# Kernel tuning notes

Hardware: AMD Instinct MI355X
Metric: run time of the kernel (lower is better)

The kernel has to match this reference:

```python
import jax, jax.numpy as jnp
import numpy as np

DEPTH_REF = jnp.array([28.01, 16.32], dtype=jnp.float32)
DIM_REF = jnp.array([[3.88, 1.63, 1.53], [0.84, 1.76, 0.66], [1.78, 1.52, 1.78]], dtype=jnp.float32)
TOPK = 50
DET_THRESHOLD = 0.25
PI = 3.14159265358979


def nms_hm(heat, kernel=3):
    # 3x3 max-pool NMS: keep peaks, zero everything else
    pad = (kernel - 1) // 2
    hmax = jax.lax.reduce_window(heat, -jnp.inf, jax.lax.max,
                                 (1, 1, kernel, kernel), (1, 1, 1, 1),
                                 [(0, 0), (0, 0), (pad, pad), (pad, pad)])
    return jnp.where(hmax == heat, heat, 0.0)


def select_topk(heat, K):
    B, C, H, W = heat.shape
    scores_all, inds_all = jax.lax.top_k(heat.reshape(B, C, H * W), K)  # [B,C,K]
    ys_all = (inds_all // W).astype(jnp.float32)
    xs_all = (inds_all % W).astype(jnp.float32)
    scores, inds = jax.lax.top_k(scores_all.reshape(B, C * K), K)       # [B,K] over classes
    clses = (inds // K).astype(jnp.float32)
    topk_inds = jnp.take_along_axis(inds_all.reshape(B, C * K), inds, axis=1)
    ys = jnp.take_along_axis(ys_all.reshape(B, C * K), inds, axis=1)
    xs = jnp.take_along_axis(xs_all.reshape(B, C * K), inds, axis=1)
    return scores, topk_inds, clses, ys, xs


def select_point_of_interest(index, feature_maps):
    B, Cf, H, W = feature_maps.shape
    fm = feature_maps.transpose(0, 2, 3, 1).reshape(B, H * W, Cf)
    return jnp.take_along_axis(fm, index[:, :, None], axis=1)  # [B,K,Cf]


def encode_box3d(rotys, dims, locs):
    # dims = (l, h, w); corner signs reproduce SMOKE's gather pattern
    N = rotys.shape[0]
    c, s = jnp.cos(rotys), jnp.sin(rotys)
    z, o = jnp.zeros_like(c), jnp.ones_like(c)
    ry = jnp.stack([c, z, s, z, o, z, -s, z, c], axis=1).reshape(N, 3, 3)
    sx = jnp.array([-0.5, 0.5, 0.5, 0.5, 0.5, -0.5, -0.5, -0.5], dtype=dims.dtype)
    sy = jnp.array([-1., -1., 0., 0., -1., -1., 0., 0.], dtype=dims.dtype)
    sz = jnp.array([-0.5, -0.5, -0.5, 0.5, 0.5, 0.5, 0.5, -0.5], dtype=dims.dtype)
    corners = jnp.stack([dims[:, 0:1] * sx, dims[:, 1:2] * sy, dims[:, 2:3] * sz], axis=1)  # [N,3,8]
    return jnp.einsum('nij,njk->nik', ry, corners) + locs[:, :, None]


def setup_inputs() -> dict:
    key = jax.random.key(0)
    k1, k2 = jax.random.split(key)
    B, C, H, W = 32, 3, 192, 640
    IMG_W, IMG_H = 4 * W, 4 * H
    pred_heatmap = jax.random.uniform(k1, (B, C, H, W), dtype=jnp.float32)
    pred_regression = jax.random.normal(k2, (B, 8, H, W), dtype=jnp.float32) * 0.5
    # affine image->heatmap (scale 1/4), invertible
    tm = jnp.array([[0.25, 0., 0.], [0., 0.25, 0.], [0., 0., 1.]], dtype=jnp.float32)
    trans_mat = jnp.tile(tm[None], (B, 1, 1))
    Kc = jnp.array([[721.5, 0., IMG_W / 2.], [0., 721.5, IMG_H / 2.], [0., 0., 1.]], dtype=jnp.float32)
    K_mat = jnp.tile(Kc[None], (B, 1, 1))
    img_size = jnp.tile(jnp.array([[IMG_W, IMG_H]], dtype=jnp.float32), (B, 1))
    return {"pred_heatmap": pred_heatmap, "pred_regression": pred_regression,
            "trans_mat": trans_mat, "K_mat": K_mat, "img_size": img_size}


def reference(pred_heatmap, pred_regression, trans_mat, K_mat, img_size):
    B = pred_heatmap.shape[0]
    heat = nms_hm(pred_heatmap)
    scores, inds, clses, ys, xs = select_topk(heat, TOPK)
    reg = select_point_of_interest(inds, pred_regression).reshape(-1, 8)  # [B*K,8]

    points = jnp.stack([xs.reshape(-1), ys.reshape(-1)], axis=1)          # heatmap coords
    depth_off, proj_off = reg[:, 0], reg[:, 1:3]
    dim_off, ori = reg[:, 3:6], reg[:, 6:8]
    cls_idx = clses.reshape(-1).astype(jnp.int32)

    obj_id = jnp.repeat(jnp.arange(B), TOPK)
    tm_inv = jnp.linalg.inv(trans_mat)[obj_id]   # [N,3,3]
    K_inv = jnp.linalg.inv(K_mat)[obj_id]

    # decode location: heatmap -> image -> camera frame
    proj = points + proj_off
    proj_ext = jnp.concatenate([proj, jnp.ones_like(proj[:, :1])], axis=1)
    proj_img = jnp.einsum('nij,nj->ni', tm_inv, proj_ext)                 # image-plane homog coords
    depths = depth_off * DEPTH_REF[1] + DEPTH_REF[0]
    locs = jnp.einsum('nij,nj->ni', K_inv, proj_img * depths[:, None])

    dims = jnp.exp(dim_off) * DIM_REF[cls_idx]                            # (l,h,w)
    locs = locs.at[:, 1].add(dims[:, 1] / 2)

    # decode orientation
    eps = 1e-7
    rays = jnp.arctan(locs[:, 0] / (locs[:, 2] + eps))
    alphas = jnp.arctan(ori[:, 0] / (ori[:, 1] + eps))
    alphas = jnp.where(ori[:, 1] >= 0, alphas - PI / 2, alphas + PI / 2)
    rotys = alphas + rays
    wrap = lambda a: jnp.where(a > PI, a - 2 * PI, jnp.where(a < -PI, a + 2 * PI, a))
    rotys, alphas = wrap(rotys), wrap(alphas)

    # encode 2D boxes from projected 3D corners
    corners = encode_box3d(rotys, dims, locs)                             # [N,3,8]
    proj2 = jnp.einsum('nij,njk->nik', K_mat[obj_id], corners)
    xy = proj2[:, :2] / proj2[:, 2:3]
    Wi, Hi = img_size[obj_id, 0], img_size[obj_id, 1]
    xmins = jnp.clip(xy[:, 0].min(axis=1), 0.0, Wi)
    ymins = jnp.clip(xy[:, 1].min(axis=1), 0.0, Hi)
    xmaxs = jnp.clip(xy[:, 0].max(axis=1), 0.0, Wi)
    ymaxs = jnp.clip(xy[:, 1].max(axis=1), 0.0, Hi)
    box2d = jnp.stack([xmins, ymins, xmaxs, ymaxs], axis=1)

    dims_rolled = jnp.roll(dims, -1, axis=1)                              # (h,w,l)
    result = jnp.concatenate([
        cls_idx.astype(jnp.float32)[:, None], alphas[:, None], box2d,
        dims_rolled, locs, rotys[:, None], scores.reshape(-1, 1)], axis=1)  # [B*K,14]
    keep = result[:, -1] > DET_THRESHOLD
    return jnp.where(keep[:, None], result, 0.0)
```

## Files before the change

kernel.cpp:

```cpp
#include <hip/hip_runtime.h>
#include <math.h>

#define Hd 192
#define Wd 640
#define HWp (Hd * Wd)
#define NCLS 3
#define KTOP 50
#define NB 32
#define NPL (NB * NCLS)
#define GPR 160
#define GPP (HWp / 4)
#define SPR 40
#define SEGBLK 30
#define SEGCAP 64
#define CAP 2048
#define RBK 256
#define PI_F 3.14159265358979f

__device__ inline float fmax3(float a, float b, float c) {
  return fmaxf(fmaxf(a, b), c);
}

template <typename F>
__device__ inline void peaks_in_group(const float* __restrict__ p, int g, F&& f) {
  const int y = g / GPR;
  const int x0 = (g - y * GPR) * 4;
  const float* rm = p + y * Wd + x0;
  const float4 mq = *(const float4*)rm;
  const float ml = (x0 > 0) ? rm[-1] : -INFINITY;
  const float mr = (x0 + 4 < Wd) ? rm[4] : -INFINITY;
  float4 tq; float tl, tr;
  if (y > 0) {
    const float* rt = rm - Wd;
    tq = *(const float4*)rt;
    tl = (x0 > 0) ? rt[-1] : -INFINITY;
    tr = (x0 + 4 < Wd) ? rt[4] : -INFINITY;
  } else {
    tq.x = tq.y = tq.z = tq.w = -INFINITY; tl = -INFINITY; tr = -INFINITY;
  }
  float4 bq; float bl, br;
  if (y < Hd - 1) {
    const float* rb = rm + Wd;
    bq = *(const float4*)rb;
    bl = (x0 > 0) ? rb[-1] : -INFINITY;
    br = (x0 + 4 < Wd) ? rb[4] : -INFINITY;
  } else {
    bq.x = bq.y = bq.z = bq.w = -INFINITY; bl = -INFINITY; br = -INFINITY;
  }
  const float c0 = fmax3(tl, ml, bl);
  const float c1 = fmax3(tq.x, mq.x, bq.x);
  const float c2 = fmax3(tq.y, mq.y, bq.y);
  const float c3 = fmax3(tq.z, mq.z, bq.z);
  const float c4 = fmax3(tq.w, mq.w, bq.w);
  const float c5 = fmax3(tr, mr, br);
  const int base = y * Wd + x0;
  if (mq.x == fmax3(c0, c1, c2)) f(__float_as_uint(mq.x), base + 0);
  if (mq.y == fmax3(c1, c2, c3)) f(__float_as_uint(mq.y), base + 1);
  if (mq.z == fmax3(c2, c3, c4)) f(__float_as_uint(mq.z), base + 2);
  if (mq.w == fmax3(c3, c4, c5)) f(__float_as_uint(mq.w), base + 3);
}

template <typename F>
__device__ inline void for_each_peak_plane(const float* __restrict__ p, int tid,
                                           int nth, F&& f) {
  for (int g = tid; g < GPP; g += nth) peaks_in_group(p, g, f);
}

__device__ inline unsigned long long mk_key(unsigned int bits, int idx) {
  return ((unsigned long long)bits << 32) | (unsigned int)~idx;
}

__device__ inline int bucket_of(unsigned int bits) {
  const unsigned int base = __float_as_uint(0.995f);
  if (bits <= base) return 0;
  unsigned int d = (bits - base) >> 9;
  return d > 255u ? 255 : (int)d;
}

struct Row16 {
  float4 q0, q1, q2, q3;
  float l, r;
};

__device__ inline Row16 load_row16(const float* __restrict__ rp, int x0, bool valid) {
  Row16 o;
  if (valid) {
    o.q0 = *(const float4*)(rp);
    o.q1 = *(const float4*)(rp + 4);
    o.q2 = *(const float4*)(rp + 8);
    o.q3 = *(const float4*)(rp + 12);
    o.l = (x0 > 0) ? rp[-1] : -INFINITY;
    o.r = (x0 + 16 < Wd) ? rp[16] : -INFINITY;
  } else {
    o.q0.x = o.q0.y = o.q0.z = o.q0.w = -INFINITY;
    o.q1 = o.q0; o.q2 = o.q0; o.q3 = o.q0;
    o.l = -INFINITY; o.r = -INFINITY;
  }
  return o;
}

__device__ inline float4 max3v(const float4 a, const float4 b, const float4 c) {
  float4 o;
  o.x = fmax3(a.x, b.x, c.x);
  o.y = fmax3(a.y, b.y, c.y);
  o.z = fmax3(a.z, b.z, c.z);
  o.w = fmax3(a.w, b.w, c.w);
  return o;
}

__global__ __launch_bounds__(256) void scan_kernel(
    const float* __restrict__ heat,
    int* __restrict__ counts,
    unsigned long long* __restrict__ segkey) {
  const int blk = blockIdx.x;
  const int plane = blk / SEGBLK;
  const int sub = blk - plane * SEGBLK;
  __shared__ unsigned long long s_k[SEGCAP];
  __shared__ int s_n;
  if (threadIdx.x == 0) s_n = 0;
  __syncthreads();

  const int strip = sub * 256 + threadIdx.x;
  const int y = strip / SPR;
  const int x0 = (strip - y * SPR) * 16;
  const float* pm = heat + (size_t)plane * HWp + y * Wd + x0;

  const Row16 m = load_row16(pm, x0, true);
  const Row16 t = load_row16(pm - Wd, x0, y > 0);
  const Row16 b = load_row16(pm + Wd, x0, y < Hd - 1);

  const float cl = fmax3(t.l, m.l, b.l);
  const float cr = fmax3(t.r, m.r, b.r);
  const float4 c0 = max3v(t.q0, m.q0, b.q0);
  const float4 c1 = max3v(t.q1, m.q1, b.q1);
  const float4 c2 = max3v(t.q2, m.q2, b.q2);
  const float4 c3 = max3v(t.q3, m.q3, b.q3);

  const float TH = 0.995f;
  const int base = y * Wd + x0;
#define EMIT(V, W0, W1, W2, J)                                         \
  if ((V) >= TH && (V) == fmax3((W0), (W1), (W2))) {                   \
    int slot = atomicAdd(&s_n, 1);                                     \
    if (slot < SEGCAP) s_k[slot] = mk_key(__float_as_uint(V), base + (J)); \
  }
  EMIT(m.q0.x, cl,   c0.x, c0.y, 0)
  EMIT(m.q0.y, c0.x, c0.y, c0.z, 1)
  EMIT(m.q0.z, c0.y, c0.z, c0.w, 2)
  EMIT(m.q0.w, c0.z, c0.w, c1.x, 3)
  EMIT(m.q1.x, c0.w, c1.x, c1.y, 4)
  EMIT(m.q1.y, c1.x, c1.y, c1.z, 5)
  EMIT(m.q1.z, c1.y, c1.z, c1.w, 6)
  EMIT(m.q1.w, c1.z, c1.w, c2.x, 7)
  EMIT(m.q2.x, c1.w, c2.x, c2.y, 8)
  EMIT(m.q2.y, c2.x, c2.y, c2.z, 9)
  EMIT(m.q2.z, c2.y, c2.z, c2.w, 10)
  EMIT(m.q2.w, c2.z, c2.w, c3.x, 11)
  EMIT(m.q3.x, c2.w, c3.x, c3.y, 12)
  EMIT(m.q3.y, c3.x, c3.y, c3.z, 13)
  EMIT(m.q3.z, c3.y, c3.z, c3.w, 14)
  EMIT(m.q3.w, c3.z, c3.w, cr,   15)
#undef EMIT

  __syncthreads();
  const int n = s_n;
  if (threadIdx.x == 0) counts[blk] = n;
  const int nn = n < SEGCAP ? n : SEGCAP;
  if (threadIdx.x < nn)
    segkey[(size_t)blk * SEGCAP + threadIdx.x] = s_k[threadIdx.x];
}

__device__ inline void inv3(const float* m, float* o) {
  float a = m[0], b = m[1], c = m[2];
  float d = m[3], e = m[4], f = m[5];
  float g = m[6], h = m[7], i = m[8];
  float A = e * i - f * h;
  float B = -(d * i - f * g);
  float C = d * h - e * g;
  float det = a * A + b * B + c * C;
  float id = 1.0f / det;
  o[0] = A * id;            o[1] = -(b * i - c * h) * id; o[2] = (b * f - c * e) * id;
  o[3] = B * id;            o[4] = (a * i - c * g) * id;  o[5] = -(a * f - c * d) * id;
  o[6] = C * id;            o[7] = -(a * h - b * g) * id; o[8] = (a * e - b * d) * id;
}

__device__ inline float wrap_pi(float a) {
  if (a > PI_F) return a - 2.0f * PI_F;
  if (a < -PI_F) return a + 2.0f * PI_F;
  return a;
}

__constant__ float DIM_REF_C[9] = {3.88f, 1.63f, 1.53f,
                                   0.84f, 1.76f, 0.66f,
                                   1.78f, 1.52f, 1.78f};

__global__ __launch_bounds__(768) void rank3_decode_kernel(
    const float* __restrict__ heat,
    const int* __restrict__ counts,
    const unsigned long long* __restrict__ segkey,
    const float* __restrict__ regr,
    const float* __restrict__ trans_mat,
    const float* __restrict__ K_mat,
    const float* __restrict__ img_size,
    float* __restrict__ out) {
  const int b = blockIdx.x;
  const int tid = threadIdx.x;
  const int g = tid >> 8;
  const int t = tid & 255;

  __shared__ unsigned long long s_key[NCLS][CAP];
  __shared__ unsigned long long g_key[NCLS][CAP];
  __shared__ int s_off[NCLS][SEGBLK + 1];
  __shared__ int cnt[NCLS][RBK], suf[NCLS][RBK], cur[NCLS][RBK];
  __shared__ unsigned int fb_hist[1024];
  __shared__ float cls_sc[NCLS * KTOP];
  __shared__ int cls_pi[NCLS * KTOP];
  __shared__ int sel[KTOP];
  __shared__ int s_flag[NCLS], s_M[NCLS], s_fast[NCLS], s_all_fast;
  __shared__ int fb_cnt, fb_B, fb_above, fb_T;

  const int plane = b * NCLS + g;

  if (tid == 0) s_all_fast = 1;
  if (t == 0) { s_flag[g] = 0; s_off[g][0] = 0; }
  __syncthreads();
  if (t < SEGBLK) {
    int n = counts[plane * SEGBLK + t];
    if (n > SEGCAP) { atomicOr(&s_flag[g], 1); n = SEGCAP; }
    s_off[g][t + 1] = n;
  }
  __syncthreads();
  if (t == 0) {
    int acc = 0;
    for (int i = 1; i <= SEGBLK; ++i) { acc += s_off[g][i]; s_off[g][i] = acc; }
    s_M[g] = acc;
    const int fast = (s_flag[g] == 0) && (acc >= KTOP) && (acc <= CAP);
    s_fast[g] = fast;
    if (!fast) s_all_fast = 0;
  }
  __syncthreads();

  if (s_all_fast) {
    const unsigned long long* pk = segkey + (size_t)plane * SEGBLK * SEGCAP;
    for (int i = t; i < SEGBLK * SEGCAP; i += 256) {
      const int s = i >> 6;
      const int j = i & (SEGCAP - 1);
      const int o = s_off[g][s];
      const int n = s_off[g][s + 1] - o;
      if (j < n) s_key[g][o + j] = pk[(size_t)s * SEGCAP + j];
    }
  } else {
    for (int p = 0; p < NCLS; ++p) {
      if (s_fast[p]) {
        const unsigned long long* pk =
            segkey + (size_t)(b * NCLS + p) * SEGBLK * SEGCAP;
        for (int i = tid; i < SEGBLK * SEGCAP; i += 768) {
          const int s = i >> 6;
          const int j = i & (SEGCAP - 1);
          const int o = s_off[p][s];
          const int n = s_off[p][s + 1] - o;
          if (j < n) s_key[p][o + j] = pk[(size_t)s * SEGCAP + j];
        }
        __syncthreads();
      } else {
        const float* hp = heat + (size_t)(b * NCLS + p) * HWp;
        for (int i = tid; i < 1024; i += 768) fb_hist[i] = 0;
        __syncthreads();
        for_each_peak_plane(hp, tid, 768, [&](unsigned int bits, int idx) {
          unsigned int bkt = bits >> 20; if (bkt > 1023u) bkt = 1023u;
          atomicAdd(&fb_hist[bkt], 1u);
        });
        __syncthreads();
        if (tid == 0) {
          int acc = 0, Bs = -1;
          for (int bkt = 1023; bkt >= 0; --bkt) {
            int cc = (int)fb_hist[bkt];
            if (acc + cc >= KTOP) { Bs = bkt; fb_above = acc; break; }
            acc += cc;
          }
          fb_B = Bs;
          if (Bs < 0) fb_above = acc;
        }
        __syncthreads();
        const int Bs = fb_B;
        unsigned int T;
        if (Bs < 0) {
          T = 0;
        } else {
          for (int i = tid; i < 1024; i += 768) fb_hist[i] = 0;
          __syncthreads();
          for_each_peak_plane(hp, tid, 768, [&](unsigned int bits, int idx) {
            unsigned int bkt = bits >> 20; if (bkt > 1023u) bkt = 1023u;
            if ((int)bkt == Bs) atomicAdd(&fb_hist[(bits >> 10) & 1023], 1u);
          });
          __syncthreads();
          if (tid == 0) {
            int acc = fb_above, Ss = 0;
            for (int sb = 1023; sb >= 0; --sb) {
              int cc = (int)fb_hist[sb];
              if (acc + cc >= KTOP) { Ss = sb; break; }
              acc += cc;
            }
            fb_T = (int)(((unsigned int)Bs << 20) | ((unsigned int)Ss << 10));
          }
          __syncthreads();
          T = (unsigned int)fb_T;
        }
        if (tid == 0) fb_cnt = 0;
        __syncthreads();
        for_each_peak_plane(hp, tid, 768, [&](unsigned int bits, int idx) {
          if (bits >= T) {
            int slot = atomicAdd(&fb_cnt, 1);
            if (slot < CAP) s_key[p][slot] = mk_key(bits, idx);
          }
        });
        __syncthreads();
        if (tid == 0) s_M[p] = fb_cnt < CAP ? fb_cnt : CAP;
        __syncthreads();
      }
    }
  }
  __syncthreads();
  const int M = s_M[g];

  for (int i = t; i < RBK; i += 256) { cnt[g][i] = 0; cur[g][i] = 0; }
  __syncthreads();
  for (int i = t; i < M; i += 256)
    atomicAdd(&cnt[g][bucket_of((unsigned int)(s_key[g][i] >> 32))], 1);
  __syncthreads();
  if (t == 0) {
    int acc = 0;
    for (int bq = RBK - 1; bq >= 0; --bq) { suf[g][bq] = acc; acc += cnt[g][bq]; }
  }
  __syncthreads();
  for (int i = t; i < M; i += 256) {
    const unsigned long long k = s_key[g][i];
    const int bq = bucket_of((unsigned int)(k >> 32));
    const int slot = suf[g][bq] + atomicAdd(&cur[g][bq], 1);
    g_key[g][slot] = k;
  }
  __syncthreads();
  for (int i = t; i < M; i += 256) {
    const unsigned long long k = g_key[g][i];
    const int bq = bucket_of((unsigned int)(k >> 32));
    const int st = suf[g][bq];
    const int nb = cnt[g][bq];
    int rank = st;
    for (int tt = st; tt < st + nb; ++tt) rank += (g_key[g][tt] > k);
    if (rank < KTOP) {
      cls_sc[g * KTOP + rank] = __uint_as_float((unsigned int)(k >> 32));
      cls_pi[g * KTOP + rank] = (int)~((unsigned int)k);
    }
  }
  for (int s2 = M + t; s2 < KTOP; s2 += 256) {
    cls_sc[g * KTOP + s2] = 0.0f;
    cls_pi[g * KTOP + s2] = 0;
  }
  __syncthreads();

  if (tid < NCLS * KTOP) {
    const float v = cls_sc[tid];
    int rank = 0;
    for (int j = 0; j < NCLS * KTOP; ++j) {
      const float w = cls_sc[j];
      rank += (w > v) || (w == v && j < tid);
    }
    if (rank < KTOP) sel[rank] = tid;
  }
  __syncthreads();

  if (tid < KTOP) {
    const int i = sel[tid];
    const int cls = i / KTOP;
    const float score = cls_sc[i];
    const int ind = cls_pi[i];
    const float ys = (float)(ind / Wd);
    const float xs = (float)(ind - (ind / Wd) * Wd);

    const float* rb = regr + (size_t)b * 8 * HWp + ind;
    const float r0 = rb[0 * HWp], r1 = rb[1 * HWp], r2 = rb[2 * HWp], r3 = rb[3 * HWp];
    const float r4 = rb[4 * HWp], r5 = rb[5 * HWp], r6 = rb[6 * HWp], r7 = rb[7 * HWp];

    float tm[9], km[9], tmi[9], kmi[9];
#pragma unroll
    for (int q = 0; q < 9; ++q) { tm[q] = trans_mat[b * 9 + q]; km[q] = K_mat[b * 9 + q]; }
    inv3(tm, tmi);
    inv3(km, kmi);

    const float px = xs + r1, py = ys + r2;
    const float gx = tmi[0] * px + tmi[1] * py + tmi[2];
    const float gy = tmi[3] * px + tmi[4] * py + tmi[5];
    const float gz = tmi[6] * px + tmi[7] * py + tmi[8];
    const float depth = r0 * 16.32f + 28.01f;
    const float qx = gx * depth, qy = gy * depth, qz = gz * depth;
    const float lx = kmi[0] * qx + kmi[1] * qy + kmi[2] * qz;
    float ly = kmi[3] * qx + kmi[4] * qy + kmi[5] * qz;
    const float lz = kmi[6] * qx + kmi[7] * qy + kmi[8] * qz;

    const float d0 = expf(r3) * DIM_REF_C[cls * 3 + 0];
    const float d1 = expf(r4) * DIM_REF_C[cls * 3 + 1];
    const float d2 = expf(r5) * DIM_REF_C[cls * 3 + 2];
    ly += d1 * 0.5f;

    const float ray = atanf(lx / (lz + 1e-7f));
    float alpha = atanf(r6 / (r7 + 1e-7f));
    alpha += (r7 >= 0.0f) ? -PI_F * 0.5f : PI_F * 0.5f;
    const float roty = wrap_pi(alpha + ray);
    alpha = wrap_pi(alpha);

    const float SX[8] = {-0.5f, 0.5f, 0.5f, 0.5f, 0.5f, -0.5f, -0.5f, -0.5f};
    const float SY[8] = {-1.0f, -1.0f, 0.0f, 0.0f, -1.0f, -1.0f, 0.0f, 0.0f};
    const float SZ[8] = {-0.5f, -0.5f, -0.5f, 0.5f, 0.5f, 0.5f, 0.5f, -0.5f};
    const float cr = cosf(roty), sr = sinf(roty);
    float minx = INFINITY, maxx = -INFINITY, miny = INFINITY, maxy = -INFINITY;
#pragma unroll
    for (int j = 0; j < 8; ++j) {
      const float ax = d0 * SX[j], ay = d1 * SY[j], az = d2 * SZ[j];
      const float cx = cr * ax + sr * az + lx;
      const float cy = ay + ly;
      const float cz = -sr * ax + cr * az + lz;
      const float ppx = km[0] * cx + km[1] * cy + km[2] * cz;
      const float ppy = km[3] * cx + km[4] * cy + km[5] * cz;
      const float ppz = km[6] * cx + km[7] * cy + km[8] * cz;
      const float X = ppx / ppz, Y = ppy / ppz;
      minx = fminf(minx, X); maxx = fmaxf(maxx, X);
      miny = fminf(miny, Y); maxy = fmaxf(maxy, Y);
    }
    const float Wi = img_size[b * 2 + 0], Hi = img_size[b * 2 + 1];
    const float xmin = fminf(fmaxf(minx, 0.0f), Wi);
    const float ymin = fminf(fmaxf(miny, 0.0f), Hi);
    const float xmax = fminf(fmaxf(maxx, 0.0f), Wi);
    const float ymax = fminf(fmaxf(maxy, 0.0f), Hi);

    float* o = out + (size_t)(b * KTOP + tid) * 14;
    if (score > 0.25f) {
      o[0] = (float)cls; o[1] = alpha;
      o[2] = xmin; o[3] = ymin; o[4] = xmax; o[5] = ymax;
      o[6] = d1; o[7] = d2; o[8] = d0;
      o[9] = lx; o[10] = ly; o[11] = lz;
      o[12] = roty; o[13] = score;
    } else {
#pragma unroll
      for (int q = 0; q < 14; ++q) o[q] = 0.0f;
    }
  }
}


extern "C" void kernel_launch(void* const* d_in, const int* in_sizes, int n_in,
                              void* d_out, int out_size, void* d_ws, size_t ws_size,
                              hipStream_t stream) {
  const float* heat = (const float*)d_in[0];
  const float* regr = (const float*)d_in[1];
  const float* tmat = (const float*)d_in[2];
  const float* kmat = (const float*)d_in[3];
  const float* isz = (const float*)d_in[4];

  char* ws = (char*)d_ws;
  int* counts = (int*)ws;
  unsigned long long* segkey = (unsigned long long*)(ws + 16384);

  scan_kernel<<<NPL * SEGBLK, 256, 0, stream>>>(heat, counts, segkey);
  rank3_decode_kernel<<<NB, 768, 0, stream>>>(heat, counts, segkey,
                                              regr, tmat, kmat, isz,
                                              (float*)d_out);
}
```

Measured before the change: 213.4 us.

## Fuse scan and rank/decode into one kernel using last-block-done atomic counters

After: 312.2 us. 1.46x slower.

```diff
diff --git a/kernel.cpp b/kernel.cpp
--- a/kernel.cpp
+++ b/kernel.cpp
@@ -16,6 +16,35 @@
 #define CAP 2048
 #define RBK 256
 #define PI_F 3.14159265358979f
+
+#define OFF_COUNTS 0
+#define OFF_SEGKEY 16384
+#define OFF_PSC 0x200000
+#define OFF_PPI 0x206000
+#define OFF_FLAGS 0x20C000
+
+__device__ inline void g_store_u64(unsigned long long* p, unsigned long long v) {
+  __hip_atomic_store(p, v, __ATOMIC_RELAXED, __HIP_MEMORY_SCOPE_AGENT);
+}
+__device__ inline unsigned long long g_load_u64(const unsigned long long* p) {
+  return __hip_atomic_load((unsigned long long*)p, __ATOMIC_RELAXED,
+                           __HIP_MEMORY_SCOPE_AGENT);
+}
+__device__ inline void g_store_i32(int* p, int v) {
+  __hip_atomic_store(p, v, __ATOMIC_RELAXED, __HIP_MEMORY_SCOPE_AGENT);
+}
+__device__ inline int g_load_i32(const int* p) {
+  return __hip_atomic_load((int*)p, __ATOMIC_RELAXED, __HIP_MEMORY_SCOPE_AGENT);
+}
+__device__ inline void g_store_f32(float* p, float v) {
+  __hip_atomic_store(p, v, __ATOMIC_RELAXED, __HIP_MEMORY_SCOPE_AGENT);
+}
+__device__ inline float g_load_f32(const float* p) {
+  return __hip_atomic_load((float*)p, __ATOMIC_RELAXED, __HIP_MEMORY_SCOPE_AGENT);
+}
+__device__ inline int done_add_acqrel(int* p) {
+  return __hip_atomic_fetch_add(p, 1, __ATOMIC_ACQ_REL, __HIP_MEMORY_SCOPE_AGENT);
+}
 
 __device__ inline float fmax3(float a, float b, float c) {
   return fmaxf(fmaxf(a, b), c);
@@ -108,67 +137,6 @@
   return o;
 }
 
-__global__ __launch_bounds__(256) void scan_kernel(
-    const float* __restrict__ heat,
-    int* __restrict__ counts,
-    unsigned long long* __restrict__ segkey) {
-  const int blk = blockIdx.x;
-  const int plane = blk / SEGBLK;
-  const int sub = blk - plane * SEGBLK;
-  __shared__ unsigned long long s_k[SEGCAP];
-  __shared__ int s_n;
-  if (threadIdx.x == 0) s_n = 0;
-  __syncthreads();
-
-  const int strip = sub * 256 + threadIdx.x;
-  const int y = strip / SPR;
-  const int x0 = (strip - y * SPR) * 16;
-  const float* pm = heat + (size_t)plane * HWp + y * Wd + x0;
-
-  const Row16 m = load_row16(pm, x0, true);
-  const Row16 t = load_row16(pm - Wd, x0, y > 0);
-  const Row16 b = load_row16(pm + Wd, x0, y < Hd - 1);
-
-  const float cl = fmax3(t.l, m.l, b.l);
-  const float cr = fmax3(t.r, m.r, b.r);
-  const float4 c0 = max3v(t.q0, m.q0, b.q0);
-  const float4 c1 = max3v(t.q1, m.q1, b.q1);
-  const float4 c2 = max3v(t.q2, m.q2, b.q2);
-  const float4 c3 = max3v(t.q3, m.q3, b.q3);
-
-  const float TH = 0.995f;
-  const int base = y * Wd + x0;
-#define EMIT(V, W0, W1, W2, J)                                         \
-  if ((V) >= TH && (V) == fmax3((W0), (W1), (W2))) {                   \
-    int slot = atomicAdd(&s_n, 1);                                     \
-    if (slot < SEGCAP) s_k[slot] = mk_key(__float_as_uint(V), base + (J)); \
-  }
-  EMIT(m.q0.x, cl,   c0.x, c0.y, 0)
-  EMIT(m.q0.y, c0.x, c0.y, c0.z, 1)
-  EMIT(m.q0.z, c0.y, c0.z, c0.w, 2)
-  EMIT(m.q0.w, c0.z, c0.w, c1.x, 3)
-  EMIT(m.q1.x, c0.w, c1.x, c1.y, 4)
-  EMIT(m.q1.y, c1.x, c1.y, c1.z, 5)
-  EMIT(m.q1.z, c1.y, c1.z, c1.w, 6)
-  EMIT(m.q1.w, c1.z, c1.w, c2.x, 7)
-  EMIT(m.q2.x, c1.w, c2.x, c2.y, 8)
-  EMIT(m.q2.y, c2.x, c2.y, c2.z, 9)
-  EMIT(m.q2.z, c2.y, c2.z, c2.w, 10)
-  EMIT(m.q2.w, c2.z, c2.w, c3.x, 11)
-  EMIT(m.q3.x, c2.w, c3.x, c3.y, 12)
-  EMIT(m.q3.y, c3.x, c3.y, c3.z, 13)
-  EMIT(m.q3.z, c3.y, c3.z, c3.w, 14)
-  EMIT(m.q3.w, c3.z, c3.w, cr,   15)
-#undef EMIT
-
-  __syncthreads();
-  const int n = s_n;
-  if (threadIdx.x == 0) counts[blk] = n;
-  const int nn = n < SEGCAP ? n : SEGCAP;
-  if (threadIdx.x < nn)
-    segkey[(size_t)blk * SEGCAP + threadIdx.x] = s_k[threadIdx.x];
-}
-
 __device__ inline void inv3(const float* m, float* o) {
   float a = m[0], b = m[1], c = m[2];
   float d = m[3], e = m[4], f = m[5];
@@ -193,175 +161,257 @@
                                    0.84f, 1.76f, 0.66f,
                                    1.78f, 1.52f, 1.78f};
 
-__global__ __launch_bounds__(768) void rank3_decode_kernel(
+__global__ __launch_bounds__(128) void zero_flags_kernel(int* __restrict__ flags) {
+  flags[threadIdx.x] = 0;
+}
+
+__global__ __launch_bounds__(256) void fused_kernel(
     const float* __restrict__ heat,
-    const int* __restrict__ counts,
-    const unsigned long long* __restrict__ segkey,
     const float* __restrict__ regr,
     const float* __restrict__ trans_mat,
     const float* __restrict__ K_mat,
     const float* __restrict__ img_size,
+    int* __restrict__ counts,
+    unsigned long long* __restrict__ segkey,
+    float* __restrict__ plane_sc,
+    int* __restrict__ plane_pi,
+    int* __restrict__ plane_done,
+    int* __restrict__ batch_done,
     float* __restrict__ out) {
-  const int b = blockIdx.x;
+  const int blk = blockIdx.x;
+  const int plane = blk % NPL;
+  const int sub = blk / NPL;
   const int tid = threadIdx.x;
-  const int g = tid >> 8;
-  const int t = tid & 255;
-
-  __shared__ unsigned long long s_key[NCLS][CAP];
-  __shared__ unsigned long long g_key[NCLS][CAP];
-  __shared__ int s_off[NCLS][SEGBLK + 1];
-  __shared__ int cnt[NCLS][RBK], suf[NCLS][RBK], cur[NCLS][RBK];
-  __shared__ unsigned int fb_hist[1024];
-  __shared__ float cls_sc[NCLS * KTOP];
-  __shared__ int cls_pi[NCLS * KTOP];
+
+  __shared__ unsigned long long s_key[CAP];
+  __shared__ unsigned long long c_key[CAP];
+  __shared__ unsigned long long s_k[SEGCAP];
+  __shared__ int s_off[SEGBLK + 1];
+  __shared__ int cnt[RBK], suf[RBK], cur[RBK];
+  __shared__ float d_sc[NCLS * KTOP];
+  __shared__ int d_pi[NCLS * KTOP];
   __shared__ int sel[KTOP];
-  __shared__ int s_flag[NCLS], s_M[NCLS], s_fast[NCLS], s_all_fast;
-  __shared__ int fb_cnt, fb_B, fb_above, fb_T;
-
-  const int plane = b * NCLS + g;
-
-  if (tid == 0) s_all_fast = 1;
-  if (t == 0) { s_flag[g] = 0; s_off[g][0] = 0; }
-  __syncthreads();
-  if (t < SEGBLK) {
-    int n = counts[plane * SEGBLK + t];
-    if (n > SEGCAP) { atomicOr(&s_flag[g], 1); n = SEGCAP; }
-    s_off[g][t + 1] = n;
-  }
-  __syncthreads();
-  if (t == 0) {
+  __shared__ int s_n, s_flag, s_M, s_fast, s_win, s_last;
+  __shared__ int s_fbB, s_fbAbove, s_fbT, s_fbCnt;
+
+  if (tid == 0) s_n = 0;
+  __syncthreads();
+
+  {
+    const int strip = sub * 256 + tid;
+    const int y = strip / SPR;
+    const int x0 = (strip - y * SPR) * 16;
+    const float* pm = heat + (size_t)plane * HWp + y * Wd + x0;
+
+    const Row16 m = load_row16(pm, x0, true);
+    const Row16 t = load_row16(pm - Wd, x0, y > 0);
+    const Row16 bt = load_row16(pm + Wd, x0, y < Hd - 1);
+
+    const float cl = fmax3(t.l, m.l, bt.l);
+    const float cr = fmax3(t.r, m.r, bt.r);
+    const float4 c0 = max3v(t.q0, m.q0, bt.q0);
+    const float4 c1 = max3v(t.q1, m.q1, bt.q1);
+    const float4 c2 = max3v(t.q2, m.q2, bt.q2);
+    const float4 c3 = max3v(t.q3, m.q3, bt.q3);
+
+    const float TH = 0.995f;
+    const int base = y * Wd + x0;
+#define EMIT(V, W0, W1, W2, J)                                         \
+    if ((V) >= TH && (V) == fmax3((W0), (W1), (W2))) {                 \
+      int slot = atomicAdd(&s_n, 1);                                   \
+      if (slot < SEGCAP) s_k[slot] = mk_key(__float_as_uint(V), base + (J)); \
+    }
+    EMIT(m.q0.x, cl,   c0.x, c0.y, 0)
+    EMIT(m.q0.y, c0.x, c0.y, c0.z, 1)
+    EMIT(m.q0.z, c0.y, c0.z, c0.w, 2)
+    EMIT(m.q0.w, c0.z, c0.w, c1.x, 3)
+    EMIT(m.q1.x, c0.w, c1.x, c1.y, 4)
+    EMIT(m.q1.y, c1.x, c1.y, c1.z, 5)
+    EMIT(m.q1.z, c1.y, c1.z, c1.w, 6)
+    EMIT(m.q1.w, c1.z, c1.w, c2.x, 7)
+    EMIT(m.q2.x, c1.w, c2.x, c2.y, 8)
+    EMIT(m.q2.y, c2.x, c2.y, c2.z, 9)
+    EMIT(m.q2.z, c2.y, c2.z, c2.w, 10)
+    EMIT(m.q2.w, c2.z, c2.w, c3.x, 11)
+    EMIT(m.q3.x, c2.w, c3.x, c3.y, 12)
+    EMIT(m.q3.y, c3.x, c3.y, c3.z, 13)
+    EMIT(m.q3.z, c3.y, c3.z, c3.w, 14)
+    EMIT(m.q3.w, c3.z, c3.w, cr,   15)
+#undef EMIT
+  }
+
+  __syncthreads();
+  {
+    const int n = s_n;
+    const int cidx = plane * SEGBLK + sub;
+    if (tid == 0) g_store_i32(&counts[cidx], n);
+    const int nn = n < SEGCAP ? n : SEGCAP;
+    if (tid < nn)
+      g_store_u64(&segkey[(size_t)cidx * SEGCAP + tid], s_k[tid]);
+  }
+  __syncthreads();
+  if (tid == 0) {
+    const int r = done_add_acqrel(&plane_done[plane]);
+    s_win = (r == SEGBLK - 1);
+  }
+  __syncthreads();
+  if (!s_win) return;
+
+  if (tid == 0) { s_flag = 0; s_off[0] = 0; }
+  __syncthreads();
+  if (tid < SEGBLK) {
+    int nv = g_load_i32(&counts[plane * SEGBLK + tid]);
+    if (nv > SEGCAP) { atomicOr(&s_flag, 1); nv = SEGCAP; }
+    s_off[tid + 1] = nv;
+  }
+  __syncthreads();
+  if (tid == 0) {
     int acc = 0;
-    for (int i = 1; i <= SEGBLK; ++i) { acc += s_off[g][i]; s_off[g][i] = acc; }
-    s_M[g] = acc;
-    const int fast = (s_flag[g] == 0) && (acc >= KTOP) && (acc <= CAP);
-    s_fast[g] = fast;
-    if (!fast) s_all_fast = 0;
-  }
-  __syncthreads();
-
-  if (s_all_fast) {
+    for (int i = 1; i <= SEGBLK; ++i) { acc += s_off[i]; s_off[i] = acc; }
+    s_M = acc;
+    s_fast = (s_flag == 0) && (acc >= KTOP) && (acc <= CAP);
+  }
+  __syncthreads();
+
+  if (s_fast) {
     const unsigned long long* pk = segkey + (size_t)plane * SEGBLK * SEGCAP;
-    for (int i = t; i < SEGBLK * SEGCAP; i += 256) {
-      const int s = i >> 6;
+    for (int i = tid; i < SEGBLK * SEGCAP; i += 256) {
+      const int sg = i >> 6;
       const int j = i & (SEGCAP - 1);
-      const int o = s_off[g][s];
-      const int n = s_off[g][s + 1] - o;
-      if (j < n) s_key[g][o + j] = pk[(size_t)s * SEGCAP + j];
-    }
+      const int o = s_off[sg];
+      const int nsg = s_off[sg + 1] - o;
+      if (j < nsg) s_key[o + j] = g_load_u64(&pk[i]);
+    }
+    __syncthreads();
   } else {
-    for (int p = 0; p < NCLS; ++p) {
-      if (s_fast[p]) {
-        const unsigned long long* pk =
-            segkey + (size_t)(b * NCLS + p) * SEGBLK * SEGCAP;
-        for (int i = tid; i < SEGBLK * SEGCAP; i += 768) {
-          const int s = i >> 6;
-          const int j = i & (SEGCAP - 1);
-          const int o = s_off[p][s];
-          const int n = s_off[p][s + 1] - o;
-          if (j < n) s_key[p][o + j] = pk[(size_t)s * SEGCAP + j];
+    const float* hp = heat + (size_t)plane * HWp;
+    unsigned int* fb_hist = (unsigned int*)c_key;
+    for (int i = tid; i < 1024; i += 256) fb_hist[i] = 0;
+    __syncthreads();
+    for_each_peak_plane(hp, tid, 256, [&](unsigned int bits, int idx) {
+      unsigned int bkt = bits >> 20; if (bkt > 1023u) bkt = 1023u;
+      atomicAdd(&fb_hist[bkt], 1u);
+    });
+    __syncthreads();
+    if (tid == 0) {
+      int acc = 0, Bs = -1;
+      for (int bkt = 1023; bkt >= 0; --bkt) {
+        int cc = (int)fb_hist[bkt];
+        if (acc + cc >= KTOP) { Bs = bkt; s_fbAbove = acc; break; }
+        acc += cc;
+      }
+      s_fbB = Bs;
+      if (Bs < 0) s_fbAbove = acc;
+    }
+    __syncthreads();
+    const int Bs = s_fbB;
+    unsigned int T;
+    if (Bs < 0) {
+      T = 0;
+    } else {
+      for (int i = tid; i < 1024; i += 256) fb_hist[i] = 0;
+      __syncthreads();
+      for_each_peak_plane(hp, tid, 256, [&](unsigned int bits, int idx) {
+        unsigned int bkt = bits >> 20; if (bkt > 1023u) bkt = 1023u;
+        if ((int)bkt == Bs) atomicAdd(&fb_hist[(bits >> 10) & 1023], 1u);
+      });
+      __syncthreads();
+      if (tid == 0) {
+        int acc = s_fbAbove, Ss = 0;
+        for (int sb = 1023; sb >= 0; --sb) {
+          int cc = (int)fb_hist[sb];
+          if (acc + cc >= KTOP) { Ss = sb; break; }
+          acc += cc;
         }
-        __syncthreads();
-      } else {
-        const float* hp = heat + (size_t)(b * NCLS + p) * HWp;
-        for (int i = tid; i < 1024; i += 768) fb_hist[i] = 0;
-        __syncthreads();
-        for_each_peak_plane(hp, tid, 768, [&](unsigned int bits, int idx) {
-          unsigned int bkt = bits >> 20; if (bkt > 1023u) bkt = 1023u;
-          atomicAdd(&fb_hist[bkt], 1u);
-        });
-        __syncthreads();
-        if (tid == 0) {
-          int acc = 0, Bs = -1;
-          for (int bkt = 1023; bkt >= 0; --bkt) {
-            int cc = (int)fb_hist[bkt];
-            if (acc + cc >= KTOP) { Bs = bkt; fb_above = acc; break; }
-            acc += cc;
-          }
-          fb_B = Bs;
-          if (Bs < 0) fb_above = acc;
-        }
-        __syncthreads();
-        const int Bs = fb_B;
-        unsigned int T;
-        if (Bs < 0) {
-          T = 0;
-        } else {
-          for (int i = tid; i < 1024; i += 768) fb_hist[i] = 0;
-          __syncthreads();
-          for_each_peak_plane(hp, tid, 768, [&](unsigned int bits, int idx) {
-            unsigned int bkt = bits >> 20; if (bkt > 1023u) bkt = 1023u;
-            if ((int)bkt == Bs) atomicAdd(&fb_hist[(bits >> 10) & 1023], 1u);
-          });
-          __syncthreads();
-          if (tid == 0) {
-            int acc = fb_above, Ss = 0;
-            for (int sb = 1023; sb >= 0; --sb) {
-              int cc = (int)fb_hist[sb];
-              if (acc + cc >= KTOP) { Ss = sb; break; }
-              acc += cc;
-            }
-            fb_T = (int)(((unsigned int)Bs << 20) | ((unsigned int)Ss << 10));
-          }
-          __syncthreads();
-          T = (unsigned int)fb_T;
-        }
-        if (tid == 0) fb_cnt = 0;
-        __syncthreads();
-        for_each_peak_plane(hp, tid, 768, [&](unsigned int bits, int idx) {
-          if (bits >= T) {
-            int slot = atomicAdd(&fb_cnt, 1);
-            if (slot < CAP) s_key[p][slot] = mk_key(bits, idx);
-          }
-        });
-        __syncthreads();
-        if (tid == 0) s_M[p] = fb_cnt < CAP ? fb_cnt : CAP;
-        __syncthreads();
+        s_fbT = (int)(((unsigned int)Bs << 20) | ((unsigned int)Ss << 10));
       }
-    }
-  }
-  __syncthreads();
-  const int M = s_M[g];
-
-  for (int i = t; i < RBK; i += 256) { cnt[g][i] = 0; cur[g][i] = 0; }
-  __syncthreads();
-  for (int i = t; i < M; i += 256)
-    atomicAdd(&cnt[g][bucket_of((unsigned int)(s_key[g][i] >> 32))], 1);
-  __syncthreads();
-  if (t == 0) {
-    int acc = 0;
-    for (int bq = RBK - 1; bq >= 0; --bq) { suf[g][bq] = acc; acc += cnt[g][bq]; }
-  }
-  __syncthreads();
-  for (int i = t; i < M; i += 256) {
-    const unsigned long long k = s_key[g][i];
+      __syncthreads();
+      T = (unsigned int)s_fbT;
+    }
+    if (tid == 0) s_fbCnt = 0;
+    __syncthreads();
+    for_each_peak_plane(hp, tid, 256, [&](unsigned int bits, int idx) {
+      if (bits >= T) {
+        int slot = atomicAdd(&s_fbCnt, 1);
+        if (slot < CAP) s_key[slot] = mk_key(bits, idx);
+      }
+    });
+    __syncthreads();
+    if (tid == 0) s_M = s_fbCnt < CAP ? s_fbCnt : CAP;
+    __syncthreads();
+  }
+  const int M = s_M;
+
+  cnt[tid] = 0;
+  cur[tid] = 0;
+  __syncthreads();
+  for (int i = tid; i < M; i += 256)
+    atomicAdd(&cnt[bucket_of((unsigned int)(s_key[i] >> 32))], 1);
+  __syncthreads();
+  suf[tid] = cnt[tid];
+  __syncthreads();
+#pragma unroll
+  for (int d = 1; d < RBK; d <<= 1) {
+    const int v = (tid + d < RBK) ? suf[tid + d] : 0;
+    __syncthreads();
+    suf[tid] += v;
+    __syncthreads();
+  }
+  {
+    const int excl = suf[tid] - cnt[tid];
+    __syncthreads();
+    suf[tid] = excl;
+  }
+  __syncthreads();
+  for (int i = tid; i < M; i += 256) {
+    const unsigned long long k = s_key[i];
     const int bq = bucket_of((unsigned int)(k >> 32));
-    const int slot = suf[g][bq] + atomicAdd(&cur[g][bq], 1);
-    g_key[g][slot] = k;
-  }
-  __syncthreads();
-  for (int i = t; i < M; i += 256) {
-    const unsigned long long k = g_key[g][i];
-    const int bq = bucket_of((unsigned int)(k >> 32));
-    const int st = suf[g][bq];
-    const int nb = cnt[g][bq];
-    int rank = st;
-    for (int tt = st; tt < st + nb; ++tt) rank += (g_key[g][tt] > k);
-    if (rank < KTOP) {
-      cls_sc[g * KTOP + rank] = __uint_as_float((unsigned int)(k >> 32));
-      cls_pi[g * KTOP + rank] = (int)~((unsigned int)k);
-    }
-  }
-  for (int s2 = M + t; s2 < KTOP; s2 += 256) {
-    cls_sc[g * KTOP + s2] = 0.0f;
-    cls_pi[g * KTOP + s2] = 0;
-  }
-  __syncthreads();
-
+    const int slot = suf[bq] + atomicAdd(&cur[bq], 1);
+    c_key[slot] = k;
+  }
+  __syncthreads();
+  {
+    float* psc = plane_sc + plane * 64;
+    int* ppi = plane_pi + plane * 64;
+    for (int i = tid; i < M; i += 256) {
+      const unsigned long long k = c_key[i];
+      const int bq = bucket_of((unsigned int)(k >> 32));
+      const int st = suf[bq];
+      const int nb = cnt[bq];
+      int rank = st;
+      for (int tt = st; tt < st + nb; ++tt) rank += (c_key[tt] > k);
+      if (rank < KTOP) {
+        g_store_f32(&psc[rank], __uint_as_float((unsigned int)(k >> 32)));
+        g_store_i32(&ppi[rank], (int)~((unsigned int)k));
+      }
+    }
+    for (int s2 = M + tid; s2 < KTOP; s2 += 256) {
+      g_store_f32(&psc[s2], 0.0f);
+      g_store_i32(&ppi[s2], 0);
+    }
+  }
+  __syncthreads();
+  if (tid == 0) {
+    const int r = done_add_acqrel(&batch_done[plane / NCLS]);
+    s_last = (r == NCLS - 1);
+  }
+  __syncthreads();
+  if (!s_last) return;
+
+  const int b = plane / NCLS;
   if (tid < NCLS * KTOP) {
-    const float v = cls_sc[tid];
+    const int c = tid / KTOP;
+    const int k2 = tid - c * KTOP;
+    d_sc[tid] = g_load_f32(&plane_sc[(b * NCLS + c) * 64 + k2]);
+    d_pi[tid] = g_load_i32(&plane_pi[(b * NCLS + c) * 64 + k2]);
+  }
+  __syncthreads();
+
+  if (tid < NCLS * KTOP) {
+    const float v = d_sc[tid];
     int rank = 0;
     for (int j = 0; j < NCLS * KTOP; ++j) {
-      const float w = cls_sc[j];
+      const float w = d_sc[j];
       rank += (w > v) || (w == v && j < tid);
     }
     if (rank < KTOP) sel[rank] = tid;
@@ -371,8 +421,8 @@
   if (tid < KTOP) {
     const int i = sel[tid];
     const int cls = i / KTOP;
-    const float score = cls_sc[i];
-    const int ind = cls_pi[i];
+    const float score = d_sc[i];
+    const int ind = d_pi[i];
     const float ys = (float)(ind / Wd);
     const float xs = (float)(ind - (ind / Wd) * Wd);
 
@@ -456,11 +506,16 @@
   const float* isz = (const float*)d_in[4];
 
   char* ws = (char*)d_ws;
-  int* counts = (int*)ws;
-  unsigned long long* segkey = (unsigned long long*)(ws + 16384);
-
-  scan_kernel<<<NPL * SEGBLK, 256, 0, stream>>>(heat, counts, segkey);
-  rank3_decode_kernel<<<NB, 768, 0, stream>>>(heat, counts, segkey,
-                                              regr, tmat, kmat, isz,
-                                              (float*)d_out);
-}
+  int* counts = (int*)(ws + OFF_COUNTS);
+  unsigned long long* segkey = (unsigned long long*)(ws + OFF_SEGKEY);
+  float* plane_sc = (float*)(ws + OFF_PSC);
+  int* plane_pi = (int*)(ws + OFF_PPI);
+  int* plane_done = (int*)(ws + OFF_FLAGS);
+  int* batch_done = plane_done + NPL;
+
+  zero_flags_kernel<<<1, 128, 0, stream>>>(plane_done);
+  fused_kernel<<<NPL * SEGBLK, 256, 0, stream>>>(
+      heat, regr, tmat, kmat, isz,
+      counts, segkey, plane_sc, plane_pi, plane_done, batch_done,
+      (float*)d_out);
+}
```
